# Kernel tuning notes

Hardware: AMD Instinct MI355X
Metric: run time of the kernel (lower is better)

Reference implementation:

```python
import jax, jax.numpy as jnp
import numpy as np

N_HEADS = 16
N_EMB = 1024
HEAD_SIZE = 64
BLOCK_SIZE = 2048


def setup_inputs() -> dict:
    key = jax.random.key(0)
    k1, k2, k3, k4, k5 = jax.random.split(key, 5)
    B, T, E, H, D = 4, BLOCK_SIZE, N_EMB, N_HEADS, HEAD_SIZE
    s = 1.0 / np.sqrt(E)
    x = jax.random.normal(k1, (B, T, E), dtype=jnp.float32)
    # Stacked per-head projection weights (Linear with bias=False): [H, E, D]
    Wq = jax.random.normal(k2, (H, E, D), dtype=jnp.float32) * s
    Wk = jax.random.normal(k3, (H, E, D), dtype=jnp.float32) * s
    Wv = jax.random.normal(k4, (H, E, D), dtype=jnp.float32) * s
    Wo = jax.random.normal(k5, (H * D, E), dtype=jnp.float32) * (1.0 / np.sqrt(H * D))
    return {"x": x, "Wq": Wq, "Wk": Wk, "Wv": Wv, "Wo": Wo}


def reference(x, Wq, Wk, Wv, Wo):
    # x: [B,T,E]; Wq/Wk/Wv: [H,E,D]; Wo: [H*D,E]
    B, T, E = x.shape
    H, _, D = Wq.shape
    q = jnp.einsum('bte,hed->bhtd', x, Wq)
    k = jnp.einsum('bte,hed->bhtd', x, Wk)
    v = jnp.einsum('bte,hed->bhtd', x, Wv)
    scores = jnp.einsum('bhtd,bhsd->bhts', q, k) * (D ** -0.5)  # [B,H,T,T]
    causal = jnp.tril(jnp.ones((T, T), dtype=bool))
    scores = jnp.where(causal, scores, -jnp.inf)
    wei = jax.nn.softmax(scores, axis=-1)  # dropout is identity in eval mode
    out = jnp.einsum('bhts,bhsd->bhtd', wei, v)  # [B,H,T,D]
    out = out.transpose(0, 2, 1, 3).reshape(B, T, H * D)  # concat heads
    return out @ Wo  # [B,T,E]
```

## Files before the change

kernel.cpp:

```cpp
#include <hip/hip_runtime.h>

#define B_  4
#define T_  2048
#define E_  1024
#define H_  16
#define D_  64
#define HD_ 1024
#define BT_ 8192

typedef __bf16 bf16x8 __attribute__((ext_vector_type(8)));
typedef float  f32x4  __attribute__((ext_vector_type(4)));

static __device__ __forceinline__ unsigned short f2bf(float f) {
  union { float f; unsigned u; } v; v.f = f;
  unsigned r = v.u + 0x7FFFu + ((v.u >> 16) & 1u);
  return (unsigned short)(r >> 16);
}
static __device__ __forceinline__ bf16x8 ldb8(const unsigned short* p) {
  return *(const bf16x8*)p;
}

#define GLD_LDS16(gp, lp)                                                      \
  __builtin_amdgcn_global_load_lds(                                            \
      (const __attribute__((address_space(1))) void*)(gp),                     \
      (__attribute__((address_space(3))) void*)(lp), 16, 0, 0)


__global__ __launch_bounds__(256) void cast_x_k(const float* __restrict__ x,
                                                unsigned short* __restrict__ xb) {
  int i = blockIdx.x * 256 + threadIdx.x;
  float4 v = ((const float4*)x)[i];
  ushort4 o;
  o.x = f2bf(v.x); o.y = f2bf(v.y); o.z = f2bf(v.z); o.w = f2bf(v.w);
  ((ushort4*)xb)[i] = o;
}

__global__ __launch_bounds__(256) void cast_wqkv_k(const float* __restrict__ Wq,
                                                   const float* __restrict__ Wk,
                                                   const float* __restrict__ Wv,
                                                   unsigned short* __restrict__ wT) {
  int tid = blockIdx.x * 256 + threadIdx.x;
  int e = tid & (E_ - 1);
  int d = (tid >> 10) & (D_ - 1);
  int h = (tid >> 16) & (H_ - 1);
  int w = tid >> 20;
  const float* src = (w == 0) ? Wq : (w == 1) ? Wk : Wv;
  wT[tid] = f2bf(src[(h * E_ + e) * D_ + d]);
}

__global__ __launch_bounds__(256) void cast_wo_k(const float* __restrict__ Wo,
                                                 unsigned short* __restrict__ woT) {
  int tid = blockIdx.x * 256 + threadIdx.x;
  int hd = tid & (HD_ - 1);
  int e  = tid >> 10;
  woT[tid] = f2bf(Wo[hd * E_ + e]);
}

static __device__ __forceinline__ void gemm_core(const unsigned short* __restrict__ A,
                                                 const unsigned short* __restrict__ BT,
                                                 const int K, const int m0, const int n0,
                                                 unsigned short* lA, unsigned short* lB,
                                                 f32x4 acc[4][4]) {
  const int tid  = threadIdx.x;
  const int wave = tid >> 6;
  const int lane = tid & 63;
  const int wm = wave & 1, wn = wave >> 1;
  const int l16 = lane & 15, quad = lane >> 4;

  const unsigned short* gA = A + (size_t)(m0 + (tid >> 2)) * K + (tid & 3) * 8;
  const unsigned short* gB = BT + (size_t)(n0 + (tid >> 2)) * K + (tid & 3) * 8;
  unsigned short* dA0 = lA + wave * 512;
  unsigned short* dA1 = lA + 64 * 32 + wave * 512;
  unsigned short* dB0 = lB + wave * 512;
  unsigned short* dB1 = lB + 64 * 32 + wave * 512;

  #pragma unroll
  for (int i = 0; i < 4; ++i)
    #pragma unroll
    for (int j = 0; j < 4; ++j) acc[i][j] = (f32x4){0.f, 0.f, 0.f, 0.f};

  for (int kb = 0; kb < K; kb += 32) {
    GLD_LDS16(gA + kb, dA0);
    GLD_LDS16(gA + (size_t)64 * K + kb, dA1);
    GLD_LDS16(gB + kb, dB0);
    GLD_LDS16(gB + (size_t)64 * K + kb, dB1);
    __syncthreads();
    bf16x8 aF[4], bF[4];
    #pragma unroll
    for (int i = 0; i < 4; ++i)
      aF[i] = ldb8(lA + (wm * 64 + i * 16 + l16) * 32 + quad * 8);
    #pragma unroll
    for (int j = 0; j < 4; ++j)
      bF[j] = ldb8(lB + (wn * 64 + j * 16 + l16) * 32 + quad * 8);
    #pragma unroll
    for (int i = 0; i < 4; ++i)
      #pragma unroll
      for (int j = 0; j < 4; ++j)
        acc[i][j] = __builtin_amdgcn_mfma_f32_16x16x32_bf16(aF[i], bF[j], acc[i][j], 0, 0, 0);
    __syncthreads();
  }
}

__global__ __launch_bounds__(256) void qkv_gemm_k(const unsigned short* __restrict__ xb,
                                                  const unsigned short* __restrict__ wT,
                                                  unsigned short* __restrict__ q,
                                                  unsigned short* __restrict__ k,
                                                  unsigned short* __restrict__ vT) {
  __shared__ unsigned short lA[128 * 32], lB[128 * 32];
  f32x4 acc[4][4];
  const int m0 = blockIdx.x * 128, n0 = blockIdx.y * 128;
  gemm_core(xb, wT, E_, m0, n0, lA, lB, acc);

  const int wave = threadIdx.x >> 6, lane = threadIdx.x & 63;
  const int wm = wave & 1, wn = wave >> 1;
  const int l16 = lane & 15, quad = lane >> 4;
  #pragma unroll
  for (int i = 0; i < 4; ++i) {
    #pragma unroll
    for (int j = 0; j < 4; ++j) {
      const int n = n0 + wn * 64 + j * 16 + l16;
      const int type = n >> 10, h = (n >> 6) & 15, d = n & 63;
      #pragma unroll
      for (int r = 0; r < 4; ++r) {
        const int m = m0 + wm * 64 + i * 16 + quad * 4 + r;
        const int b = m >> 11, t = m & (T_ - 1);
        const unsigned short val = f2bf(acc[i][j][r]);
        if (type == 0)      q[((size_t)(b * H_ + h) * T_ + t) * D_ + d] = val;
        else if (type == 1) k[((size_t)(b * H_ + h) * T_ + t) * D_ + d] = val;
        else                vT[((size_t)(b * H_ + h) * D_ + d) * T_ + t] = val;
      }
    }
  }
}

__global__ __launch_bounds__(256) void proj_k(const unsigned short* __restrict__ ao,
                                              const unsigned short* __restrict__ woT,
                                              float* __restrict__ out) {
  __shared__ unsigned short lA[128 * 32], lB[128 * 32];
  f32x4 acc[4][4];
  const int m0 = blockIdx.x * 128, n0 = blockIdx.y * 128;
  gemm_core(ao, woT, HD_, m0, n0, lA, lB, acc);

  const int wave = threadIdx.x >> 6, lane = threadIdx.x & 63;
  const int wm = wave & 1, wn = wave >> 1;
  const int l16 = lane & 15, quad = lane >> 4;
  #pragma unroll
  for (int i = 0; i < 4; ++i)
    #pragma unroll
    for (int j = 0; j < 4; ++j)
      #pragma unroll
      for (int r = 0; r < 4; ++r)
        out[(size_t)(m0 + wm * 64 + i * 16 + quad * 4 + r) * E_ +
            n0 + wn * 64 + j * 16 + l16] = acc[i][j][r];
}

__global__ __launch_bounds__(256) void attn_k(const unsigned short* __restrict__ q,
                                              const unsigned short* __restrict__ k,
                                              const unsigned short* __restrict__ vT,
                                              unsigned short* __restrict__ ao) {
  __shared__ unsigned short lK[64 * 64];
  __shared__ unsigned short lV[64 * 64];
  __shared__ unsigned short lP[4][32][72];
  const int tid  = threadIdx.x;
  const int lane = tid & 63;
  const int wave = tid >> 6;
  const int l16  = lane & 15;
  const int quad = lane >> 4;
  const int h = blockIdx.y, b = blockIdx.z;
  const size_t bh = (size_t)(b * H_ + h);
  const unsigned short* qp = q  + bh * (T_ * D_);
  const unsigned short* kp = k  + bh * (T_ * D_);
  const unsigned short* vp = vT + bh * (D_ * T_);
  const float C = 0.18033688011112042f;

  const int srow = tid >> 3;
  const int sseg = tid & 7;
  const int kseg = sseg ^ (srow & 7);
  unsigned short* dK0 = lK + wave * 512;
  unsigned short* dK1 = lK + 2048 + wave * 512;
  unsigned short* dV0 = lV + wave * 512;
  unsigned short* dV1 = lV + 2048 + wave * 512;
  const int sw = (l16 & 7);

  #pragma unroll
  for (int pr = 0; pr < 2; ++pr) {
    const int qblk = (pr == 0) ? (int)blockIdx.x : 15 - (int)blockIdx.x;
    const int q0 = qblk * 128 + wave * 32;

    bf16x8 aq[2][2];
    #pragma unroll
    for (int rb = 0; rb < 2; ++rb)
      #pragma unroll
      for (int hh = 0; hh < 2; ++hh)
        aq[rb][hh] = ldb8(qp + (q0 + rb * 16 + l16) * D_ + hh * 32 + quad * 8);

    float lr[2][4];
    f32x4 o[2][4];
    #pragma unroll
    for (int rb = 0; rb < 2; ++rb) {
      #pragma unroll
      for (int r = 0; r < 4; ++r) lr[rb][r] = 0.f;
      #pragma unroll
      for (int nb = 0; nb < 4; ++nb) o[rb][nb] = (f32x4){0.f, 0.f, 0.f, 0.f};
    }

    const int nch = 2 * (qblk + 1);
    for (int c = 0; c < nch; ++c) {
      const int s0 = c * 64;
      GLD_LDS16(kp + (s0 + srow) * D_ + kseg * 8, dK0);
      GLD_LDS16(kp + (s0 + 32 + srow) * D_ + kseg * 8, dK1);
      GLD_LDS16(vp + (size_t)srow * T_ + s0 + kseg * 8, dV0);
      GLD_LDS16(vp + (size_t)(32 + srow) * T_ + s0 + kseg * 8, dV1);
      __syncthreads();
      if (s0 <= q0 + 31) {
        f32x4 sc[2][4];
        #pragma unroll
        for (int rb = 0; rb < 2; ++rb)
          #pragma unroll
          for (int j = 0; j < 4; ++j) sc[rb][j] = (f32x4){0.f, 0.f, 0.f, 0.f};
        #pragma unroll
        for (int j = 0; j < 4; ++j) {
          const int r = j * 16 + l16;
          bf16x8 bk0 = ldb8(lK + r * 64 + ((quad ^ sw) << 3));
          bf16x8 bk1 = ldb8(lK + r * 64 + (((4 + quad) ^ sw) << 3));
          #pragma unroll
          for (int rb = 0; rb < 2; ++rb) {
            sc[rb][j] = __builtin_amdgcn_mfma_f32_16x16x32_bf16(aq[rb][0], bk0, sc[rb][j], 0, 0, 0);
            sc[rb][j] = __builtin_amdgcn_mfma_f32_16x16x32_bf16(aq[rb][1], bk1, sc[rb][j], 0, 0, 0);
          }
        }
        const bool domask = (s0 + 63 > q0);
        #pragma unroll
        for (int rb = 0; rb < 2; ++rb) {
          #pragma unroll
          for (int j = 0; j < 4; ++j) {
            #pragma unroll
            for (int r = 0; r < 4; ++r) {
              float p = __builtin_amdgcn_exp2f(sc[rb][j][r] * C);
              if (domask) {
                const int qg = q0 + rb * 16 + quad * 4 + r;
                if (s0 + j * 16 + l16 > qg) p = 0.f;
              }
              sc[rb][j][r] = p;
              lr[rb][r] += p;
            }
          }
        }
        #pragma unroll
        for (int rb = 0; rb < 2; ++rb)
          #pragma unroll
          for (int j = 0; j < 4; ++j)
            #pragma unroll
            for (int r = 0; r < 4; ++r)
              lP[wave][rb * 16 + quad * 4 + r][j * 16 + l16] = f2bf(sc[rb][j][r]);
        __builtin_amdgcn_wave_barrier();
        bf16x8 aP[2][2];
        #pragma unroll
        for (int rb = 0; rb < 2; ++rb)
          #pragma unroll
          for (int hh = 0; hh < 2; ++hh)
            aP[rb][hh] = ldb8(&lP[wave][rb * 16 + l16][hh * 32 + quad * 8]);
        __builtin_amdgcn_wave_barrier();
        #pragma unroll
        for (int nb = 0; nb < 4; ++nb) {
          const int d = nb * 16 + l16;
          bf16x8 bV0 = ldb8(lV + d * 64 + ((quad ^ sw) << 3));
          bf16x8 bV1 = ldb8(lV + d * 64 + (((4 + quad) ^ sw) << 3));
          #pragma unroll
          for (int rb = 0; rb < 2; ++rb) {
            o[rb][nb] = __builtin_amdgcn_mfma_f32_16x16x32_bf16(aP[rb][0], bV0, o[rb][nb], 0, 0, 0);
            o[rb][nb] = __builtin_amdgcn_mfma_f32_16x16x32_bf16(aP[rb][1], bV1, o[rb][nb], 0, 0, 0);
          }
        }
      }
      __syncthreads();
    }

    #pragma unroll
    for (int off = 1; off < 16; off <<= 1)
      #pragma unroll
      for (int rb = 0; rb < 2; ++rb)
        #pragma unroll
        for (int r = 0; r < 4; ++r)
          lr[rb][r] += __shfl_xor(lr[rb][r], off, 64);
    #pragma unroll
    for (int rb = 0; rb < 2; ++rb) {
      #pragma unroll
      for (int r = 0; r < 4; ++r) {
        const float inv = 1.0f / lr[rb][r];
        const int t = q0 + rb * 16 + quad * 4 + r;
        #pragma unroll
        for (int nb = 0; nb < 4; ++nb)
          ao[((size_t)(b * T_ + t) * H_ + h) * D_ + nb * 16 + l16] = f2bf(o[rb][nb][r] * inv);
      }
    }
  }
}


extern "C" void kernel_launch(void* const* d_in, const int* in_sizes, int n_in,
                              void* d_out, int out_size, void* d_ws, size_t ws_size,
                              hipStream_t stream) {
  const float* x  = (const float*)d_in[0];
  const float* Wq = (const float*)d_in[1];
  const float* Wk = (const float*)d_in[2];
  const float* Wv = (const float*)d_in[3];
  const float* Wo = (const float*)d_in[4];
  float* out = (float*)d_out;

  char* ws = (char*)d_ws;
  unsigned short* xb   = (unsigned short*)(ws + 0);
  unsigned short* wT   = (unsigned short*)(ws + 16777216);
  unsigned short* woT  = (unsigned short*)(ws + 23068672);
  unsigned short* qb   = (unsigned short*)(ws + 25165824);
  unsigned short* kb   = (unsigned short*)(ws + 41943040);
  unsigned short* vTb  = (unsigned short*)(ws + 58720256);
  unsigned short* aob  = (unsigned short*)(ws + 75497472);

  cast_x_k<<<dim3((BT_ * E_) / 4 / 256), dim3(256), 0, stream>>>(x, xb);
  cast_wqkv_k<<<dim3((3 * H_ * D_ * E_) / 256), dim3(256), 0, stream>>>(Wq, Wk, Wv, wT);
  cast_wo_k<<<dim3((E_ * HD_) / 256), dim3(256), 0, stream>>>(Wo, woT);
  qkv_gemm_k<<<dim3(BT_ / 128, 3072 / 128), dim3(256), 0, stream>>>(xb, wT, qb, kb, vTb);
  attn_k<<<dim3(8, H_, B_), dim3(256), 0, stream>>>(qb, kb, vTb, aob);
  proj_k<<<dim3(BT_ / 128, E_ / 128), dim3(256), 0, stream>>>(aob, woT, out);
}
```

Measured before the change: 296.4 us.

## Process paired causal query blocks together sharing K/V tile loads

The attention kernel now handles its low and high query blocks in one pass over the K/V chunks instead of two sequential passes. Each K/V tile loaded into LDS feeds both blocks, roughly halving K/V global traffic and barrier rounds for the shared prefix. The softmax scale is folded into Q in the QKV GEMM epilogue, and bf16 conversion uses the native cast. The cost is about twice the register state per wave (two sets of accumulators, Q fragments and P tiles), a larger LDS P buffer, and some branch overhead.

```diff
diff --git a/kernel.cpp b/kernel.cpp
--- a/kernel.cpp
+++ b/kernel.cpp
@@ -12,9 +12,8 @@
 typedef float  f32x4  __attribute__((ext_vector_type(4)));
 
 static __device__ __forceinline__ unsigned short f2bf(float f) {
-  union { float f; unsigned u; } v; v.f = f;
-  unsigned r = v.u + 0x7FFFu + ((v.u >> 16) & 1u);
-  return (unsigned short)(r >> 16);
+  __bf16 h = (__bf16)f;
+  return __builtin_bit_cast(unsigned short, h);
 }
 static __device__ __forceinline__ bf16x8 ldb8(const unsigned short* p) {
   return *(const bf16x8*)p;
@@ -114,20 +113,24 @@
   const int wave = threadIdx.x >> 6, lane = threadIdx.x & 63;
   const int wm = wave & 1, wn = wave >> 1;
   const int l16 = lane & 15, quad = lane >> 4;
+  const int type = n0 >> 10;
+  const float C = 0.18033688011112042f;
   #pragma unroll
   for (int i = 0; i < 4; ++i) {
     #pragma unroll
     for (int j = 0; j < 4; ++j) {
       const int n = n0 + wn * 64 + j * 16 + l16;
-      const int type = n >> 10, h = (n >> 6) & 15, d = n & 63;
+      const int h = (n >> 6) & 15, d = n & 63;
       #pragma unroll
       for (int r = 0; r < 4; ++r) {
         const int m = m0 + wm * 64 + i * 16 + quad * 4 + r;
         const int b = m >> 11, t = m & (T_ - 1);
-        const unsigned short val = f2bf(acc[i][j][r]);
-        if (type == 0)      q[((size_t)(b * H_ + h) * T_ + t) * D_ + d] = val;
-        else if (type == 1) k[((size_t)(b * H_ + h) * T_ + t) * D_ + d] = val;
-        else                vT[((size_t)(b * H_ + h) * D_ + d) * T_ + t] = val;
+        if (type == 0)
+          q[((size_t)(b * H_ + h) * T_ + t) * D_ + d] = f2bf(acc[i][j][r] * C);
+        else if (type == 1)
+          k[((size_t)(b * H_ + h) * T_ + t) * D_ + d] = f2bf(acc[i][j][r]);
+        else
+          vT[((size_t)(b * H_ + h) * D_ + d) * T_ + t] = f2bf(acc[i][j][r]);
       }
     }
   }
@@ -160,7 +163,7 @@
                                               unsigned short* __restrict__ ao) {
   __shared__ unsigned short lK[64 * 64];
   __shared__ unsigned short lV[64 * 64];
-  __shared__ unsigned short lP[4][32][72];
+  __shared__ unsigned short lP[4][2][32][72];
   const int tid  = threadIdx.x;
   const int lane = tid & 63;
   const int wave = tid >> 6;
@@ -171,130 +174,171 @@
   const unsigned short* qp = q  + bh * (T_ * D_);
   const unsigned short* kp = k  + bh * (T_ * D_);
   const unsigned short* vp = vT + bh * (D_ * T_);
-  const float C = 0.18033688011112042f;
 
   const int srow = tid >> 3;
-  const int sseg = tid & 7;
-  const int kseg = sseg ^ (srow & 7);
+  const int kseg = (tid & 7) ^ (srow & 7);
   unsigned short* dK0 = lK + wave * 512;
   unsigned short* dK1 = lK + 2048 + wave * 512;
   unsigned short* dV0 = lV + wave * 512;
   unsigned short* dV1 = lV + 2048 + wave * 512;
   const int sw = (l16 & 7);
 
-  #pragma unroll
-  for (int pr = 0; pr < 2; ++pr) {
-    const int qblk = (pr == 0) ? (int)blockIdx.x : 15 - (int)blockIdx.x;
-    const int q0 = qblk * 128 + wave * 32;
-
-    bf16x8 aq[2][2];
-    #pragma unroll
-    for (int rb = 0; rb < 2; ++rb)
-      #pragma unroll
-      for (int hh = 0; hh < 2; ++hh)
-        aq[rb][hh] = ldb8(qp + (q0 + rb * 16 + l16) * D_ + hh * 32 + quad * 8);
-
-    float lr[2][4];
-    f32x4 o[2][4];
-    #pragma unroll
-    for (int rb = 0; rb < 2; ++rb) {
-      #pragma unroll
-      for (int r = 0; r < 4; ++r) lr[rb][r] = 0.f;
-      #pragma unroll
-      for (int nb = 0; nb < 4; ++nb) o[rb][nb] = (f32x4){0.f, 0.f, 0.f, 0.f};
-    }
-
-    const int nch = 2 * (qblk + 1);
-    for (int c = 0; c < nch; ++c) {
-      const int s0 = c * 64;
-      GLD_LDS16(kp + (s0 + srow) * D_ + kseg * 8, dK0);
-      GLD_LDS16(kp + (s0 + 32 + srow) * D_ + kseg * 8, dK1);
-      GLD_LDS16(vp + (size_t)srow * T_ + s0 + kseg * 8, dV0);
-      GLD_LDS16(vp + (size_t)(32 + srow) * T_ + s0 + kseg * 8, dV1);
-      __syncthreads();
-      if (s0 <= q0 + 31) {
-        f32x4 sc[2][4];
+  const int xb_ = (int)blockIdx.x;
+  const int q0L = xb_ * 128 + wave * 32;
+  const int q0H = (15 - xb_) * 128 + wave * 32;
+  const int nchL = 2 * (xb_ + 1);
+  const int nchH = 2 * (16 - xb_);
+
+  bf16x8 aqL[2][2], aqH[2][2];
+  #pragma unroll
+  for (int rb = 0; rb < 2; ++rb)
+    #pragma unroll
+    for (int hh = 0; hh < 2; ++hh) {
+      aqL[rb][hh] = ldb8(qp + (q0L + rb * 16 + l16) * D_ + hh * 32 + quad * 8);
+      aqH[rb][hh] = ldb8(qp + (q0H + rb * 16 + l16) * D_ + hh * 32 + quad * 8);
+    }
+
+  float lrL[2][4], lrH[2][4];
+  f32x4 oL[2][4], oH[2][4];
+  #pragma unroll
+  for (int rb = 0; rb < 2; ++rb) {
+    #pragma unroll
+    for (int r = 0; r < 4; ++r) { lrL[rb][r] = 0.f; lrH[rb][r] = 0.f; }
+    #pragma unroll
+    for (int nb = 0; nb < 4; ++nb) {
+      oL[rb][nb] = (f32x4){0.f, 0.f, 0.f, 0.f};
+      oH[rb][nb] = (f32x4){0.f, 0.f, 0.f, 0.f};
+    }
+  }
+
+  for (int c = 0; c < nchH; ++c) {
+    const int s0 = c * 64;
+    GLD_LDS16(kp + (s0 + srow) * D_ + kseg * 8, dK0);
+    GLD_LDS16(kp + (s0 + 32 + srow) * D_ + kseg * 8, dK1);
+    GLD_LDS16(vp + (size_t)srow * T_ + s0 + kseg * 8, dV0);
+    GLD_LDS16(vp + (size_t)(32 + srow) * T_ + s0 + kseg * 8, dV1);
+    __syncthreads();
+    const bool aH = (s0 <= q0H + 31);
+    const bool aL = (c < nchL) && (s0 <= q0L + 31);
+    if (aH || aL) {
+      f32x4 scH[2][4], scL[2][4];
+      #pragma unroll
+      for (int rb = 0; rb < 2; ++rb)
+        #pragma unroll
+        for (int j = 0; j < 4; ++j) {
+          scH[rb][j] = (f32x4){0.f, 0.f, 0.f, 0.f};
+          scL[rb][j] = (f32x4){0.f, 0.f, 0.f, 0.f};
+        }
+      #pragma unroll
+      for (int j = 0; j < 4; ++j) {
+        const int sr = j * 16 + l16;
+        bf16x8 bk0 = ldb8(lK + sr * 64 + ((quad ^ sw) << 3));
+        bf16x8 bk1 = ldb8(lK + sr * 64 + (((4 + quad) ^ sw) << 3));
+        if (aH) {
+          #pragma unroll
+          for (int rb = 0; rb < 2; ++rb) {
+            scH[rb][j] = __builtin_amdgcn_mfma_f32_16x16x32_bf16(aqH[rb][0], bk0, scH[rb][j], 0, 0, 0);
+            scH[rb][j] = __builtin_amdgcn_mfma_f32_16x16x32_bf16(aqH[rb][1], bk1, scH[rb][j], 0, 0, 0);
+          }
+        }
+        if (aL) {
+          #pragma unroll
+          for (int rb = 0; rb < 2; ++rb) {
+            scL[rb][j] = __builtin_amdgcn_mfma_f32_16x16x32_bf16(aqL[rb][0], bk0, scL[rb][j], 0, 0, 0);
+            scL[rb][j] = __builtin_amdgcn_mfma_f32_16x16x32_bf16(aqL[rb][1], bk1, scL[rb][j], 0, 0, 0);
+          }
+        }
+      }
+      if (aH) {
+        const bool mH = (s0 + 63 > q0H);
         #pragma unroll
         for (int rb = 0; rb < 2; ++rb)
           #pragma unroll
-          for (int j = 0; j < 4; ++j) sc[rb][j] = (f32x4){0.f, 0.f, 0.f, 0.f};
-        #pragma unroll
-        for (int j = 0; j < 4; ++j) {
-          const int r = j * 16 + l16;
-          bf16x8 bk0 = ldb8(lK + r * 64 + ((quad ^ sw) << 3));
-          bf16x8 bk1 = ldb8(lK + r * 64 + (((4 + quad) ^ sw) << 3));
-          #pragma unroll
-          for (int rb = 0; rb < 2; ++rb) {
-            sc[rb][j] = __builtin_amdgcn_mfma_f32_16x16x32_bf16(aq[rb][0], bk0, sc[rb][j], 0, 0, 0);
-            sc[rb][j] = __builtin_amdgcn_mfma_f32_16x16x32_bf16(aq[rb][1], bk1, sc[rb][j], 0, 0, 0);
-          }
-        }
-        const bool domask = (s0 + 63 > q0);
-        #pragma unroll
-        for (int rb = 0; rb < 2; ++rb) {
-          #pragma unroll
-          for (int j = 0; j < 4; ++j) {
+          for (int j = 0; j < 4; ++j)
             #pragma unroll
             for (int r = 0; r < 4; ++r) {
-              float p = __builtin_amdgcn_exp2f(sc[rb][j][r] * C);
-              if (domask) {
-                const int qg = q0 + rb * 16 + quad * 4 + r;
-                if (s0 + j * 16 + l16 > qg) p = 0.f;
-              }
-              sc[rb][j][r] = p;
-              lr[rb][r] += p;
+              float p = __builtin_amdgcn_exp2f(scH[rb][j][r]);
+              if (mH && (s0 + j * 16 + l16 > q0H + rb * 16 + quad * 4 + r)) p = 0.f;
+              lrH[rb][r] += p;
+              lP[wave][0][rb * 16 + quad * 4 + r][j * 16 + l16] = f2bf(p);
             }
-          }
-        }
+      }
+      if (aL) {
+        const bool mL = (s0 + 63 > q0L);
         #pragma unroll
         for (int rb = 0; rb < 2; ++rb)
           #pragma unroll
           for (int j = 0; j < 4; ++j)
             #pragma unroll
-            for (int r = 0; r < 4; ++r)
-              lP[wave][rb * 16 + quad * 4 + r][j * 16 + l16] = f2bf(sc[rb][j][r]);
-        __builtin_amdgcn_wave_barrier();
-        bf16x8 aP[2][2];
+            for (int r = 0; r < 4; ++r) {
+              float p = __builtin_amdgcn_exp2f(scL[rb][j][r]);
+              if (mL && (s0 + j * 16 + l16 > q0L + rb * 16 + quad * 4 + r)) p = 0.f;
+              lrL[rb][r] += p;
+              lP[wave][1][rb * 16 + quad * 4 + r][j * 16 + l16] = f2bf(p);
+            }
+      }
+      __builtin_amdgcn_wave_barrier();
+      bf16x8 aPH[2][2], aPL[2][2];
+      if (aH)
         #pragma unroll
         for (int rb = 0; rb < 2; ++rb)
           #pragma unroll
           for (int hh = 0; hh < 2; ++hh)
-            aP[rb][hh] = ldb8(&lP[wave][rb * 16 + l16][hh * 32 + quad * 8]);
-        __builtin_amdgcn_wave_barrier();
-        #pragma unroll
-        for (int nb = 0; nb < 4; ++nb) {
-          const int d = nb * 16 + l16;
-          bf16x8 bV0 = ldb8(lV + d * 64 + ((quad ^ sw) << 3));
-          bf16x8 bV1 = ldb8(lV + d * 64 + (((4 + quad) ^ sw) << 3));
+            aPH[rb][hh] = ldb8(&lP[wave][0][rb * 16 + l16][hh * 32 + quad * 8]);
+      if (aL)
+        #pragma unroll
+        for (int rb = 0; rb < 2; ++rb)
+          #pragma unroll
+          for (int hh = 0; hh < 2; ++hh)
+            aPL[rb][hh] = ldb8(&lP[wave][1][rb * 16 + l16][hh * 32 + quad * 8]);
+      __builtin_amdgcn_wave_barrier();
+      #pragma unroll
+      for (int nb = 0; nb < 4; ++nb) {
+        const int d = nb * 16 + l16;
+        bf16x8 bV0 = ldb8(lV + d * 64 + ((quad ^ sw) << 3));
+        bf16x8 bV1 = ldb8(lV + d * 64 + (((4 + quad) ^ sw) << 3));
+        if (aH) {
           #pragma unroll
           for (int rb = 0; rb < 2; ++rb) {
-            o[rb][nb] = __builtin_amdgcn_mfma_f32_16x16x32_bf16(aP[rb][0], bV0, o[rb][nb], 0, 0, 0);
-            o[rb][nb] = __builtin_amdgcn_mfma_f32_16x16x32_bf16(aP[rb][1], bV1, o[rb][nb], 0, 0, 0);
+            oH[rb][nb] = __builtin_amdgcn_mfma_f32_16x16x32_bf16(aPH[rb][0], bV0, oH[rb][nb], 0, 0, 0);
+            oH[rb][nb] = __builtin_amdgcn_mfma_f32_16x16x32_bf16(aPH[rb][1], bV1, oH[rb][nb], 0, 0, 0);
           }
         }
-      }
-      __syncthreads();
-    }
-
-    #pragma unroll
-    for (int off = 1; off < 16; off <<= 1)
-      #pragma unroll
-      for (int rb = 0; rb < 2; ++rb)
-        #pragma unroll
-        for (int r = 0; r < 4; ++r)
-          lr[rb][r] += __shfl_xor(lr[rb][r], off, 64);
-    #pragma unroll
-    for (int rb = 0; rb < 2; ++rb) {
+        if (aL) {
+          #pragma unroll
+          for (int rb = 0; rb < 2; ++rb) {
+            oL[rb][nb] = __builtin_amdgcn_mfma_f32_16x16x32_bf16(aPL[rb][0], bV0, oL[rb][nb], 0, 0, 0);
+            oL[rb][nb] = __builtin_amdgcn_mfma_f32_16x16x32_bf16(aPL[rb][1], bV1, oL[rb][nb], 0, 0, 0);
+          }
+        }
+      }
+    }
+    __syncthreads();
+  }
+
+  #pragma unroll
+  for (int off = 1; off < 16; off <<= 1)
+    #pragma unroll
+    for (int rb = 0; rb < 2; ++rb)
       #pragma unroll
       for (int r = 0; r < 4; ++r) {
-        const float inv = 1.0f / lr[rb][r];
-        const int t = q0 + rb * 16 + quad * 4 + r;
-        #pragma unroll
-        for (int nb = 0; nb < 4; ++nb)
-          ao[((size_t)(b * T_ + t) * H_ + h) * D_ + nb * 16 + l16] = f2bf(o[rb][nb][r] * inv);
-      }
-    }
-  }
+        lrH[rb][r] += __shfl_xor(lrH[rb][r], off, 64);
+        lrL[rb][r] += __shfl_xor(lrL[rb][r], off, 64);
+      }
+  #pragma unroll
+  for (int rb = 0; rb < 2; ++rb)
+    #pragma unroll
+    for (int r = 0; r < 4; ++r) {
+      const float invH = 1.0f / lrH[rb][r];
+      const float invL = 1.0f / lrL[rb][r];
+      const int tH = q0H + rb * 16 + quad * 4 + r;
+      const int tL = q0L + rb * 16 + quad * 4 + r;
+      #pragma unroll
+      for (int nb = 0; nb < 4; ++nb) {
+        ao[((size_t)(b * T_ + tH) * H_ + h) * D_ + nb * 16 + l16] = f2bf(oH[rb][nb][r] * invH);
+        ao[((size_t)(b * T_ + tL) * H_ + h) * D_ + nb * 16 + l16] = f2bf(oL[rb][nb][r] * invL);
+      }
+    }
 }
 
 
```

Measured after the change: 375.7 us. 1.27x slower.

## Double-buffer K/V tiles in attention and fold softmax scale into Q

Applied to the files above, without the earlier changes.

The attention kernel now double-buffers its K/V LDS tiles. The next chunk's global-to-LDS loads are issued before the current chunk is computed, with one barrier per iteration instead of two. The softmax scale is folded into Q when the QKV GEMM writes its epilogue, which removes a multiply per score. Other changes: the causal mask now applies only to the last two chunks, P is written straight to LDS, the grid is flattened to 1D, and the bf16 conversion uses the native cast. The per-wave skip for fully masked chunks is dropped, so some waves now compute and zero out chunks they previously skipped. Double buffering also doubles K/V LDS use, which may lower occupancy.

```diff
diff --git a/kernel.cpp b/kernel.cpp
--- a/kernel.cpp
+++ b/kernel.cpp
@@ -12,9 +12,8 @@
 typedef float  f32x4  __attribute__((ext_vector_type(4)));
 
 static __device__ __forceinline__ unsigned short f2bf(float f) {
-  union { float f; unsigned u; } v; v.f = f;
-  unsigned r = v.u + 0x7FFFu + ((v.u >> 16) & 1u);
-  return (unsigned short)(r >> 16);
+  __bf16 h = (__bf16)f;
+  return __builtin_bit_cast(unsigned short, h);
 }
 static __device__ __forceinline__ bf16x8 ldb8(const unsigned short* p) {
   return *(const bf16x8*)p;
@@ -114,20 +113,24 @@
   const int wave = threadIdx.x >> 6, lane = threadIdx.x & 63;
   const int wm = wave & 1, wn = wave >> 1;
   const int l16 = lane & 15, quad = lane >> 4;
+  const int type = n0 >> 10;
+  const float C = 0.18033688011112042f;
   #pragma unroll
   for (int i = 0; i < 4; ++i) {
     #pragma unroll
     for (int j = 0; j < 4; ++j) {
       const int n = n0 + wn * 64 + j * 16 + l16;
-      const int type = n >> 10, h = (n >> 6) & 15, d = n & 63;
+      const int h = (n >> 6) & 15, d = n & 63;
       #pragma unroll
       for (int r = 0; r < 4; ++r) {
         const int m = m0 + wm * 64 + i * 16 + quad * 4 + r;
         const int b = m >> 11, t = m & (T_ - 1);
-        const unsigned short val = f2bf(acc[i][j][r]);
-        if (type == 0)      q[((size_t)(b * H_ + h) * T_ + t) * D_ + d] = val;
-        else if (type == 1) k[((size_t)(b * H_ + h) * T_ + t) * D_ + d] = val;
-        else                vT[((size_t)(b * H_ + h) * D_ + d) * T_ + t] = val;
+        if (type == 0)
+          q[((size_t)(b * H_ + h) * T_ + t) * D_ + d] = f2bf(acc[i][j][r] * C);
+        else if (type == 1)
+          k[((size_t)(b * H_ + h) * T_ + t) * D_ + d] = f2bf(acc[i][j][r]);
+        else
+          vT[((size_t)(b * H_ + h) * D_ + d) * T_ + t] = f2bf(acc[i][j][r]);
       }
     }
   }
@@ -158,33 +161,30 @@
                                               const unsigned short* __restrict__ k,
                                               const unsigned short* __restrict__ vT,
                                               unsigned short* __restrict__ ao) {
-  __shared__ unsigned short lK[64 * 64];
-  __shared__ unsigned short lV[64 * 64];
+  __shared__ unsigned short lK[2][64 * 64];
+  __shared__ unsigned short lV[2][64 * 64];
   __shared__ unsigned short lP[4][32][72];
   const int tid  = threadIdx.x;
   const int lane = tid & 63;
   const int wave = tid >> 6;
   const int l16  = lane & 15;
   const int quad = lane >> 4;
-  const int h = blockIdx.y, b = blockIdx.z;
+  const int id    = (int)blockIdx.x;
+  const int bhid  = id & 63;
+  const int qpair = id >> 6;
+  const int h = bhid & 15, b = bhid >> 4;
   const size_t bh = (size_t)(b * H_ + h);
   const unsigned short* qp = q  + bh * (T_ * D_);
   const unsigned short* kp = k  + bh * (T_ * D_);
   const unsigned short* vp = vT + bh * (D_ * T_);
-  const float C = 0.18033688011112042f;
 
   const int srow = tid >> 3;
-  const int sseg = tid & 7;
-  const int kseg = sseg ^ (srow & 7);
-  unsigned short* dK0 = lK + wave * 512;
-  unsigned short* dK1 = lK + 2048 + wave * 512;
-  unsigned short* dV0 = lV + wave * 512;
-  unsigned short* dV1 = lV + 2048 + wave * 512;
+  const int kseg = (tid & 7) ^ (srow & 7);
   const int sw = (l16 & 7);
 
   #pragma unroll
   for (int pr = 0; pr < 2; ++pr) {
-    const int qblk = (pr == 0) ? (int)blockIdx.x : 15 - (int)blockIdx.x;
+    const int qblk = (pr == 0) ? qpair : 15 - qpair;
     const int q0 = qblk * 128 + wave * 32;
 
     bf16x8 aq[2][2];
@@ -205,75 +205,82 @@
     }
 
     const int nch = 2 * (qblk + 1);
+
+    {
+      unsigned short* Kb = lK[0];
+      unsigned short* Vb = lV[0];
+      GLD_LDS16(kp + srow * D_ + kseg * 8, Kb + wave * 512);
+      GLD_LDS16(kp + (32 + srow) * D_ + kseg * 8, Kb + 2048 + wave * 512);
+      GLD_LDS16(vp + (size_t)srow * T_ + kseg * 8, Vb + wave * 512);
+      GLD_LDS16(vp + (size_t)(32 + srow) * T_ + kseg * 8, Vb + 2048 + wave * 512);
+    }
+
     for (int c = 0; c < nch; ++c) {
+      __syncthreads();
+      if (c + 1 < nch) {
+        const int s1 = (c + 1) * 64;
+        unsigned short* Kb = lK[(c + 1) & 1];
+        unsigned short* Vb = lV[(c + 1) & 1];
+        GLD_LDS16(kp + (s1 + srow) * D_ + kseg * 8, Kb + wave * 512);
+        GLD_LDS16(kp + (s1 + 32 + srow) * D_ + kseg * 8, Kb + 2048 + wave * 512);
+        GLD_LDS16(vp + (size_t)srow * T_ + s1 + kseg * 8, Vb + wave * 512);
+        GLD_LDS16(vp + (size_t)(32 + srow) * T_ + s1 + kseg * 8, Vb + 2048 + wave * 512);
+      }
       const int s0 = c * 64;
-      GLD_LDS16(kp + (s0 + srow) * D_ + kseg * 8, dK0);
-      GLD_LDS16(kp + (s0 + 32 + srow) * D_ + kseg * 8, dK1);
-      GLD_LDS16(vp + (size_t)srow * T_ + s0 + kseg * 8, dV0);
-      GLD_LDS16(vp + (size_t)(32 + srow) * T_ + s0 + kseg * 8, dV1);
-      __syncthreads();
-      if (s0 <= q0 + 31) {
-        f32x4 sc[2][4];
-        #pragma unroll
-        for (int rb = 0; rb < 2; ++rb)
+      const unsigned short* Kb = lK[c & 1];
+      const unsigned short* Vb = lV[c & 1];
+      f32x4 sc[2][4];
+      #pragma unroll
+      for (int rb = 0; rb < 2; ++rb)
+        #pragma unroll
+        for (int j = 0; j < 4; ++j) sc[rb][j] = (f32x4){0.f, 0.f, 0.f, 0.f};
+      #pragma unroll
+      for (int j = 0; j < 4; ++j) {
+        const int sr = j * 16 + l16;
+        bf16x8 bk0 = ldb8(Kb + sr * 64 + ((quad ^ sw) << 3));
+        bf16x8 bk1 = ldb8(Kb + sr * 64 + (((4 + quad) ^ sw) << 3));
+        #pragma unroll
+        for (int rb = 0; rb < 2; ++rb) {
+          sc[rb][j] = __builtin_amdgcn_mfma_f32_16x16x32_bf16(aq[rb][0], bk0, sc[rb][j], 0, 0, 0);
+          sc[rb][j] = __builtin_amdgcn_mfma_f32_16x16x32_bf16(aq[rb][1], bk1, sc[rb][j], 0, 0, 0);
+        }
+      }
+      const bool domask = (c == nch - 1) || (c == nch - 2);
+      #pragma unroll
+      for (int rb = 0; rb < 2; ++rb) {
+        #pragma unroll
+        for (int j = 0; j < 4; ++j) {
           #pragma unroll
-          for (int j = 0; j < 4; ++j) sc[rb][j] = (f32x4){0.f, 0.f, 0.f, 0.f};
-        #pragma unroll
-        for (int j = 0; j < 4; ++j) {
-          const int r = j * 16 + l16;
-          bf16x8 bk0 = ldb8(lK + r * 64 + ((quad ^ sw) << 3));
-          bf16x8 bk1 = ldb8(lK + r * 64 + (((4 + quad) ^ sw) << 3));
-          #pragma unroll
-          for (int rb = 0; rb < 2; ++rb) {
-            sc[rb][j] = __builtin_amdgcn_mfma_f32_16x16x32_bf16(aq[rb][0], bk0, sc[rb][j], 0, 0, 0);
-            sc[rb][j] = __builtin_amdgcn_mfma_f32_16x16x32_bf16(aq[rb][1], bk1, sc[rb][j], 0, 0, 0);
+          for (int r = 0; r < 4; ++r) {
+            float p = __builtin_amdgcn_exp2f(sc[rb][j][r]);
+            if (domask) {
+              const int qg = q0 + rb * 16 + quad * 4 + r;
+              if (s0 + j * 16 + l16 > qg) p = 0.f;
+            }
+            lr[rb][r] += p;
+            lP[wave][rb * 16 + quad * 4 + r][j * 16 + l16] = f2bf(p);
           }
         }
-        const bool domask = (s0 + 63 > q0);
+      }
+      __builtin_amdgcn_wave_barrier();
+      bf16x8 aP[2][2];
+      #pragma unroll
+      for (int rb = 0; rb < 2; ++rb)
+        #pragma unroll
+        for (int hh = 0; hh < 2; ++hh)
+          aP[rb][hh] = ldb8(&lP[wave][rb * 16 + l16][hh * 32 + quad * 8]);
+      __builtin_amdgcn_wave_barrier();
+      #pragma unroll
+      for (int nb = 0; nb < 4; ++nb) {
+        const int d = nb * 16 + l16;
+        bf16x8 bV0 = ldb8(Vb + d * 64 + ((quad ^ sw) << 3));
+        bf16x8 bV1 = ldb8(Vb + d * 64 + (((4 + quad) ^ sw) << 3));
         #pragma unroll
         for (int rb = 0; rb < 2; ++rb) {
-          #pragma unroll
-          for (int j = 0; j < 4; ++j) {
-            #pragma unroll
-            for (int r = 0; r < 4; ++r) {
-              float p = __builtin_amdgcn_exp2f(sc[rb][j][r] * C);
-              if (domask) {
-                const int qg = q0 + rb * 16 + quad * 4 + r;
-                if (s0 + j * 16 + l16 > qg) p = 0.f;
-              }
-              sc[rb][j][r] = p;
-              lr[rb][r] += p;
-            }
-          }
+          o[rb][nb] = __builtin_amdgcn_mfma_f32_16x16x32_bf16(aP[rb][0], bV0, o[rb][nb], 0, 0, 0);
+          o[rb][nb] = __builtin_amdgcn_mfma_f32_16x16x32_bf16(aP[rb][1], bV1, o[rb][nb], 0, 0, 0);
         }
-        #pragma unroll
-        for (int rb = 0; rb < 2; ++rb)
-          #pragma unroll
-          for (int j = 0; j < 4; ++j)
-            #pragma unroll
-            for (int r = 0; r < 4; ++r)
-              lP[wave][rb * 16 + quad * 4 + r][j * 16 + l16] = f2bf(sc[rb][j][r]);
-        __builtin_amdgcn_wave_barrier();
-        bf16x8 aP[2][2];
-        #pragma unroll
-        for (int rb = 0; rb < 2; ++rb)
-          #pragma unroll
-          for (int hh = 0; hh < 2; ++hh)
-            aP[rb][hh] = ldb8(&lP[wave][rb * 16 + l16][hh * 32 + quad * 8]);
-        __builtin_amdgcn_wave_barrier();
-        #pragma unroll
-        for (int nb = 0; nb < 4; ++nb) {
-          const int d = nb * 16 + l16;
-          bf16x8 bV0 = ldb8(lV + d * 64 + ((quad ^ sw) << 3));
-          bf16x8 bV1 = ldb8(lV + d * 64 + (((4 + quad) ^ sw) << 3));
-          #pragma unroll
-          for (int rb = 0; rb < 2; ++rb) {
-            o[rb][nb] = __builtin_amdgcn_mfma_f32_16x16x32_bf16(aP[rb][0], bV0, o[rb][nb], 0, 0, 0);
-            o[rb][nb] = __builtin_amdgcn_mfma_f32_16x16x32_bf16(aP[rb][1], bV1, o[rb][nb], 0, 0, 0);
-          }
-        }
-      }
-      __syncthreads();
+      }
     }
 
     #pragma unroll
@@ -321,6 +328,6 @@
   cast_wqkv_k<<<dim3((3 * H_ * D_ * E_) / 256), dim3(256), 0, stream>>>(Wq, Wk, Wv, wT);
   cast_wo_k<<<dim3((E_ * HD_) / 256), dim3(256), 0, stream>>>(Wo, woT);
   qkv_gemm_k<<<dim3(BT_ / 128, 3072 / 128), dim3(256), 0, stream>>>(xb, wT, qb, kb, vTb);
-  attn_k<<<dim3(8, H_, B_), dim3(256), 0, stream>>>(qb, kb, vTb, aob);
+  attn_k<<<dim3(512), dim3(256), 0, stream>>>(qb, kb, vTb, aob);
   proj_k<<<dim3(BT_ / 128, E_ / 128), dim3(256), 0, stream>>>(aob, woT, out);
 }
```

Result: no change. 291.2 us (-1.7%).
